# Kernel tuning notes

Measured on AMD Instinct MI355X. Metric: run time of the kernel, lower is better.

Reference implementation:

```python
import jax, jax.numpy as jnp
import numpy as np

H = 128          # hidden_dim
NC = 100000      # num_cst
NV = 100000      # num_val
E = 1600000      # num edges
EPS = 1e-5


def _layernorm(x, g, b):
    mu = x.mean(-1, keepdims=True)
    var = x.var(-1, keepdims=True)
    return (x - mu) / jnp.sqrt(var + EPS) * g + b


def setup_inputs() -> dict:
    key = jax.random.key(0)
    ks = jax.random.split(key, 16)
    s = 0.05
    return {
        "x_val": jax.random.normal(ks[0], (NV, H), jnp.float32),
        "r_cst": jax.random.normal(ks[1], (NC, H), jnp.float32),
        "cst_edges": jax.random.randint(ks[2], (2, E), 0, NC, dtype=jnp.int32),
        "LE": jax.random.randint(ks[3], (E,), 0, 2, dtype=jnp.int32),
        "PE": jax.random.randint(ks[4], (E,), 0, 2, dtype=jnp.int32),
        "num_cst": NC,
        "num_val": NV,
        # cst_send: Linear(H,H,bias) -> ReLU -> Linear(H,4H,no bias) -> LayerNorm(4H)
        "W1": jax.random.normal(ks[5], (H, H), jnp.float32) * s,
        "b1": jax.random.normal(ks[6], (H,), jnp.float32) * s,
        "W2": jax.random.normal(ks[7], (H, 4 * H), jnp.float32) * s,
        "g1": jnp.ones((4 * H,), jnp.float32),
        "bt1": jnp.zeros((4 * H,), jnp.float32),
        # val_rec: Linear(H,H,bias) -> ReLU -> Linear(H,H,no bias) -> LayerNorm(H)
        "W3": jax.random.normal(ks[8], (H, H), jnp.float32) * s,
        "b3": jax.random.normal(ks[9], (H,), jnp.float32) * s,
        "W4": jax.random.normal(ks[10], (H, H), jnp.float32) * s,
        "g2": jnp.ones((H,), jnp.float32),
        "bt2": jnp.zeros((H,), jnp.float32),
    }


def reference(x_val, r_cst, cst_edges, LE, PE, num_cst, num_val,
              W1, b1, W2, g1, bt1, W3, b3, W4, g2, bt2):
    # cst_send MLP: [NC, H] -> [NC, 4H], LayerNorm over 4H, then view as [4*NC, H]
    m = _layernorm(jnp.maximum(r_cst @ W1 + b1, 0.0) @ W2, g1, bt1)
    m = m.reshape(4 * num_cst, H)
    # each edge picks one of the 4 message slots of its constraint
    out_idx = 4 * cst_edges[0] + 2 * LE + PE   # [E]
    in_idx = cst_edges[1]                      # [E]
    msg = m[out_idx]                           # [E, H] gather
    r_val = jax.ops.segment_sum(msg, in_idx, num_segments=num_val)  # [NV, H]
    # val_rec MLP on (x_val + r_val) with residual
    h = x_val + r_val
    return _layernorm(jnp.maximum(h @ W3 + b3, 0.0) @ W4, g2, bt2) + x_val
```

## Files before the change

### kernel.cpp

```cpp
#include <hip/hip_runtime.h>
#include <hip/hip_bf16.h>

#define H 128
#define H4 512
#define BM 16
#define BM2 32

typedef __bf16 bf16x8 __attribute__((ext_vector_type(8)));
typedef float f32x4 __attribute__((ext_vector_type(4)));

__device__ inline f32x4 mfma16(bf16x8 a, bf16x8 b, f32x4 c) {
  return __builtin_amdgcn_mfma_f32_16x16x32_bf16(a, b, c, 0, 0, 0);
}

__global__ __launch_bounds__(256) void pack_kernel(const float* __restrict__ W, int K, int N,
                                                   __bf16* __restrict__ hi,
                                                   __bf16* __restrict__ lo) {
  int idx = blockIdx.x * 256 + threadIdx.x;
  int total = (N >> 4) * (K >> 5) * 64;
  if (idx >= total) return;
  int lane = idx & 63;
  int tile = idx >> 6;
  int KT = K >> 5;
  int nt = tile / KT, kt = tile - nt * KT;
  int col = nt * 16 + (lane & 15);
  int k0 = kt * 32 + (lane >> 4) * 8;
#pragma unroll
  for (int i = 0; i < 8; ++i) {
    float x = W[(long)(k0 + i) * N + col];
    __bf16 h = (__bf16)x;
    hi[(long)idx * 8 + i] = h;
    lo[(long)idx * 8 + i] = (__bf16)(x - (float)h);
  }
}

__global__ __launch_bounds__(256) void copy_kernel(const float4* __restrict__ src,
                                                   float4* __restrict__ dst, int n4) {
  int i = blockIdx.x * 256 + threadIdx.x;
  int stride = gridDim.x * 256;
  for (; i < n4; i += stride) dst[i] = src[i];
}

__device__ inline void split8(const float* p, bf16x8& hi, bf16x8& lo) {
  float4 u = *(const float4*)p, v = *(const float4*)(p + 4);
  float vals[8] = {u.x, u.y, u.z, u.w, v.x, v.y, v.z, v.w};
#pragma unroll
  for (int i = 0; i < 8; ++i) {
    __bf16 hh = (__bf16)vals[i];
    hi[i] = hh;
    lo[i] = (__bf16)(vals[i] - (float)hh);
  }
}

__global__ __launch_bounds__(256) void cst_mlp_mfma(
    const float* __restrict__ r_cst,
    const __bf16* __restrict__ W1h, const __bf16* __restrict__ W1l,
    const float* __restrict__ b1,
    const __bf16* __restrict__ W2h, const __bf16* __restrict__ W2l,
    const float* __restrict__ g1, const float* __restrict__ bt1,
    float* __restrict__ m) {
  __shared__ float As[BM2][132];
  __shared__ float Cs[BM2][132];
  __shared__ float part_s[BM2][4];
  __shared__ float part_q[BM2][4];
  __shared__ float mu_s[BM2], rs_s[BM2];

  const int tid = threadIdx.x;
  const int wave = tid >> 6, lane = tid & 63;
  const long row0 = (long)blockIdx.x * BM2;

  {
    const float4* src = (const float4*)(r_cst + row0 * H);
#pragma unroll
    for (int i = 0; i < 4; ++i) {
      int idx = tid + i * 256;
      int r = idx >> 5, c4 = idx & 31;
      *(float4*)&As[r][c4 * 4] = src[idx];
    }
  }
  __syncthreads();

  const int fr = lane & 15;
  const int fk = (lane >> 4) * 8;
  const int rowb = (lane >> 4) * 4;

  bf16x8 a_hi[2][4], a_lo[2][4];
#pragma unroll
  for (int mt = 0; mt < 2; ++mt)
#pragma unroll
    for (int kt = 0; kt < 4; ++kt) split8(&As[mt * 16 + fr][kt * 32 + fk], a_hi[mt][kt], a_lo[mt][kt]);

#pragma unroll
  for (int t = 0; t < 2; ++t) {
    const int nt = wave * 2 + t;
    f32x4 acc0 = {0.f, 0.f, 0.f, 0.f}, acc1 = {0.f, 0.f, 0.f, 0.f};
#pragma unroll
    for (int kt = 0; kt < 4; ++kt) {
      const long fi = (long)((nt * 4 + kt) * 64 + lane) * 8;
      bf16x8 bh = *(const bf16x8*)(W1h + fi);
      bf16x8 bl = *(const bf16x8*)(W1l + fi);
      acc0 = mfma16(a_hi[0][kt], bh, acc0);
      acc0 = mfma16(a_lo[0][kt], bh, acc0);
      acc0 = mfma16(a_hi[0][kt], bl, acc0);
      acc1 = mfma16(a_hi[1][kt], bh, acc1);
      acc1 = mfma16(a_lo[1][kt], bh, acc1);
      acc1 = mfma16(a_hi[1][kt], bl, acc1);
    }
    const int col = nt * 16 + fr;
    const float bb = b1[col];
#pragma unroll
    for (int r = 0; r < 4; ++r) {
      Cs[rowb + r][col] = fmaxf(acc0[r] + bb, 0.f);
      Cs[16 + rowb + r][col] = fmaxf(acc1[r] + bb, 0.f);
    }
  }
  __syncthreads();

  bf16x8 c_hi[2][4], c_lo[2][4];
#pragma unroll
  for (int mt = 0; mt < 2; ++mt)
#pragma unroll
    for (int kt = 0; kt < 4; ++kt) split8(&Cs[mt * 16 + fr][kt * 32 + fk], c_hi[mt][kt], c_lo[mt][kt]);

  f32x4 d[2][8];
  float ss[2][4], qq[2][4];
#pragma unroll
  for (int mt = 0; mt < 2; ++mt)
#pragma unroll
    for (int r = 0; r < 4; ++r) ss[mt][r] = qq[mt][r] = 0.f;

#pragma unroll
  for (int t = 0; t < 8; ++t) {
    const int nt = wave * 8 + t;
    f32x4 acc0 = {0.f, 0.f, 0.f, 0.f}, acc1 = {0.f, 0.f, 0.f, 0.f};
#pragma unroll
    for (int kt = 0; kt < 4; ++kt) {
      const long fi = (long)((nt * 4 + kt) * 64 + lane) * 8;
      bf16x8 bh = *(const bf16x8*)(W2h + fi);
      bf16x8 bl = *(const bf16x8*)(W2l + fi);
      acc0 = mfma16(c_hi[0][kt], bh, acc0);
      acc0 = mfma16(c_lo[0][kt], bh, acc0);
      acc0 = mfma16(c_hi[0][kt], bl, acc0);
      acc1 = mfma16(c_hi[1][kt], bh, acc1);
      acc1 = mfma16(c_lo[1][kt], bh, acc1);
      acc1 = mfma16(c_hi[1][kt], bl, acc1);
    }
    d[0][t] = acc0;
    d[1][t] = acc1;
#pragma unroll
    for (int r = 0; r < 4; ++r) {
      ss[0][r] += acc0[r];
      qq[0][r] += acc0[r] * acc0[r];
      ss[1][r] += acc1[r];
      qq[1][r] += acc1[r] * acc1[r];
    }
  }

#pragma unroll
  for (int mt = 0; mt < 2; ++mt)
#pragma unroll
    for (int r = 0; r < 4; ++r) {
      float s = ss[mt][r], q = qq[mt][r];
#pragma unroll
      for (int off = 1; off < 16; off <<= 1) {
        s += __shfl_xor(s, off);
        q += __shfl_xor(q, off);
      }
      if (fr == 0) {
        part_s[mt * 16 + rowb + r][wave] = s;
        part_q[mt * 16 + rowb + r][wave] = q;
      }
    }
  __syncthreads();

  if (tid < BM2) {
    float s = part_s[tid][0] + part_s[tid][1] + part_s[tid][2] + part_s[tid][3];
    float q = part_q[tid][0] + part_q[tid][1] + part_q[tid][2] + part_q[tid][3];
    float mu = s * (1.f / H4);
    mu_s[tid] = mu;
    rs_s[tid] = rsqrtf(q * (1.f / H4) - mu * mu + 1e-5f);
  }
  __syncthreads();

#pragma unroll
  for (int t = 0; t < 8; ++t) {
    const int col = (wave * 8 + t) * 16 + fr;
    const float g = g1[col], b = bt1[col];
#pragma unroll
    for (int mt = 0; mt < 2; ++mt) {
#pragma unroll
      for (int r = 0; r < 4; ++r) {
        const int row = mt * 16 + rowb + r;
        m[(row0 + row) * H4 + col] = (d[mt][t][r] - mu_s[row]) * rs_s[row] * g + b;
      }
    }
  }
}

__global__ __launch_bounds__(256) void val_mlp_mfma(
    const float* h, const float* __restrict__ x_val,
    const __bf16* __restrict__ W3h, const __bf16* __restrict__ W3l,
    const float* __restrict__ b3,
    const __bf16* __restrict__ W4h, const __bf16* __restrict__ W4l,
    const float* __restrict__ g2, const float* __restrict__ bt2,
    float* out) {
  __shared__ float As[BM2][132];
  __shared__ float Cs[BM2][132];
  __shared__ float part_s[BM2][4];
  __shared__ float part_q[BM2][4];
  __shared__ float mu_s[BM2], rs_s[BM2];

  const int tid = threadIdx.x;
  const int wave = tid >> 6, lane = tid & 63;
  const long row0 = (long)blockIdx.x * BM2;

  {
    const float4* src = (const float4*)(h + row0 * H);
#pragma unroll
    for (int i = 0; i < 4; ++i) {
      int idx = tid + i * 256;
      int r = idx >> 5, c4 = idx & 31;
      *(float4*)&As[r][c4 * 4] = src[idx];
    }
  }
  __syncthreads();

  const int fr = lane & 15;
  const int fk = (lane >> 4) * 8;
  const int rowb = (lane >> 4) * 4;

  bf16x8 a_hi[2][4], a_lo[2][4];
#pragma unroll
  for (int mt = 0; mt < 2; ++mt)
#pragma unroll
    for (int kt = 0; kt < 4; ++kt) split8(&As[mt * 16 + fr][kt * 32 + fk], a_hi[mt][kt], a_lo[mt][kt]);

#pragma unroll
  for (int t = 0; t < 2; ++t) {
    const int nt = wave * 2 + t;
    f32x4 acc0 = {0.f, 0.f, 0.f, 0.f}, acc1 = {0.f, 0.f, 0.f, 0.f};
#pragma unroll
    for (int kt = 0; kt < 4; ++kt) {
      const long fi = (long)((nt * 4 + kt) * 64 + lane) * 8;
      bf16x8 bh = *(const bf16x8*)(W3h + fi);
      bf16x8 bl = *(const bf16x8*)(W3l + fi);
      acc0 = mfma16(a_hi[0][kt], bh, acc0);
      acc0 = mfma16(a_lo[0][kt], bh, acc0);
      acc0 = mfma16(a_hi[0][kt], bl, acc0);
      acc1 = mfma16(a_hi[1][kt], bh, acc1);
      acc1 = mfma16(a_lo[1][kt], bh, acc1);
      acc1 = mfma16(a_hi[1][kt], bl, acc1);
    }
    const int col = nt * 16 + fr;
    const float bb = b3[col];
#pragma unroll
    for (int r = 0; r < 4; ++r) {
      Cs[rowb + r][col] = fmaxf(acc0[r] + bb, 0.f);
      Cs[16 + rowb + r][col] = fmaxf(acc1[r] + bb, 0.f);
    }
  }
  __syncthreads();

  bf16x8 c_hi[2][4], c_lo[2][4];
#pragma unroll
  for (int mt = 0; mt < 2; ++mt)
#pragma unroll
    for (int kt = 0; kt < 4; ++kt) split8(&Cs[mt * 16 + fr][kt * 32 + fk], c_hi[mt][kt], c_lo[mt][kt]);

  f32x4 d[2][2];
  float ss[2][4], qq[2][4];
#pragma unroll
  for (int mt = 0; mt < 2; ++mt)
#pragma unroll
    for (int r = 0; r < 4; ++r) ss[mt][r] = qq[mt][r] = 0.f;

#pragma unroll
  for (int t = 0; t < 2; ++t) {
    const int nt = wave * 2 + t;
    f32x4 acc0 = {0.f, 0.f, 0.f, 0.f}, acc1 = {0.f, 0.f, 0.f, 0.f};
#pragma unroll
    for (int kt = 0; kt < 4; ++kt) {
      const long fi = (long)((nt * 4 + kt) * 64 + lane) * 8;
      bf16x8 bh = *(const bf16x8*)(W4h + fi);
      bf16x8 bl = *(const bf16x8*)(W4l + fi);
      acc0 = mfma16(c_hi[0][kt], bh, acc0);
      acc0 = mfma16(c_lo[0][kt], bh, acc0);
      acc0 = mfma16(c_hi[0][kt], bl, acc0);
      acc1 = mfma16(c_hi[1][kt], bh, acc1);
      acc1 = mfma16(c_lo[1][kt], bh, acc1);
      acc1 = mfma16(c_hi[1][kt], bl, acc1);
    }
    d[0][t] = acc0;
    d[1][t] = acc1;
#pragma unroll
    for (int r = 0; r < 4; ++r) {
      ss[0][r] += acc0[r];
      qq[0][r] += acc0[r] * acc0[r];
      ss[1][r] += acc1[r];
      qq[1][r] += acc1[r] * acc1[r];
    }
  }

#pragma unroll
  for (int mt = 0; mt < 2; ++mt)
#pragma unroll
    for (int r = 0; r < 4; ++r) {
      float s = ss[mt][r], q = qq[mt][r];
#pragma unroll
      for (int off = 1; off < 16; off <<= 1) {
        s += __shfl_xor(s, off);
        q += __shfl_xor(q, off);
      }
      if (fr == 0) {
        part_s[mt * 16 + rowb + r][wave] = s;
        part_q[mt * 16 + rowb + r][wave] = q;
      }
    }
  __syncthreads();

  if (tid < BM2) {
    float s = part_s[tid][0] + part_s[tid][1] + part_s[tid][2] + part_s[tid][3];
    float q = part_q[tid][0] + part_q[tid][1] + part_q[tid][2] + part_q[tid][3];
    float mu = s * (1.f / H);
    mu_s[tid] = mu;
    rs_s[tid] = rsqrtf(q * (1.f / H) - mu * mu + 1e-5f);
  }
  __syncthreads();

#pragma unroll
  for (int t = 0; t < 2; ++t) {
    const int col = (wave * 2 + t) * 16 + fr;
    const float g = g2[col], b = bt2[col];
#pragma unroll
    for (int mt = 0; mt < 2; ++mt) {
#pragma unroll
      for (int r = 0; r < 4; ++r) {
        const int row = mt * 16 + rowb + r;
        const float xv = x_val[(row0 + row) * H + col];
        out[(row0 + row) * H + col] = (d[mt][t][r] - mu_s[row]) * rs_s[row] * g + b + xv;
      }
    }
  }
}

__global__ __launch_bounds__(256) void cst_mlp_kernel(
    const float* __restrict__ r_cst,
    const float* __restrict__ W1, const float* __restrict__ b1,
    const float* __restrict__ W2, const float* __restrict__ g1,
    const float* __restrict__ bt1, float* __restrict__ m) {
  __shared__ float As[BM][H];
  __shared__ float Cs[BM][H];
  __shared__ float Ds[BM][H4];
  __shared__ float mu_s[BM], rs_s[BM];
  const int tid = threadIdx.x;
  const long row0 = (long)blockIdx.x * BM;
  {
    const float4* src = (const float4*)(r_cst + row0 * H);
    float4* dst = (float4*)&As[0][0];
#pragma unroll
    for (int i = 0; i < 2; ++i) dst[tid + i * 256] = src[tid + i * 256];
  }
  __syncthreads();
  {
    const int j = tid & (H - 1);
    const int r0 = (tid >> 7) * 8;
    float acc[8] = {0, 0, 0, 0, 0, 0, 0, 0};
#pragma unroll 4
    for (int k = 0; k < H; ++k) {
      float w = W1[k * H + j];
#pragma unroll
      for (int r = 0; r < 8; ++r) acc[r] = fmaf(As[r0 + r][k], w, acc[r]);
    }
    float bb = b1[j];
#pragma unroll
    for (int r = 0; r < 8; ++r) Cs[r0 + r][j] = fmaxf(acc[r] + bb, 0.f);
  }
  __syncthreads();
  {
    const int j = tid * 2;
    float acc[BM][2];
#pragma unroll
    for (int r = 0; r < BM; ++r) acc[r][0] = acc[r][1] = 0.f;
    for (int k = 0; k < H; k += 4) {
      float4 c[BM];
#pragma unroll
      for (int r = 0; r < BM; ++r) c[r] = *(const float4*)&Cs[r][k];
#pragma unroll
      for (int kk = 0; kk < 4; ++kk) {
        const float2 w = *(const float2*)&W2[(k + kk) * H4 + j];
#pragma unroll
        for (int r = 0; r < BM; ++r) {
          float cv = (&c[r].x)[kk];
          acc[r][0] = fmaf(cv, w.x, acc[r][0]);
          acc[r][1] = fmaf(cv, w.y, acc[r][1]);
        }
      }
    }
#pragma unroll
    for (int r = 0; r < BM; ++r) {
      Ds[r][j] = acc[r][0];
      Ds[r][j + 1] = acc[r][1];
    }
  }
  __syncthreads();
  {
    const int wv = tid >> 6, lane = tid & 63;
    for (int r = wv * 4; r < wv * 4 + 4; ++r) {
      float s = 0.f, q = 0.f;
      const float4* rowp = (const float4*)&Ds[r][0];
#pragma unroll
      for (int i = 0; i < 2; ++i) {
        float4 v = rowp[lane * 2 + i];
        s += v.x + v.y + v.z + v.w;
        q += v.x * v.x + v.y * v.y + v.z * v.z + v.w * v.w;
      }
#pragma unroll
      for (int off = 32; off; off >>= 1) {
        s += __shfl_xor(s, off);
        q += __shfl_xor(q, off);
      }
      if (lane == 0) {
        float mu = s * (1.f / H4);
        mu_s[r] = mu;
        rs_s[r] = rsqrtf(q * (1.f / H4) - mu * mu + 1e-5f);
      }
    }
  }
  __syncthreads();
  {
    float4* out4 = (float4*)(m + row0 * H4);
    const float4* D4 = (const float4*)&Ds[0][0];
    const float4* g4 = (const float4*)g1;
    const float4* b4 = (const float4*)bt1;
#pragma unroll
    for (int it = 0; it < 8; ++it) {
      int e4 = tid + it * 256;
      int r = e4 >> 7;
      int c4 = e4 & 127;
      float4 v = D4[e4];
      float4 g = g4[c4], b = b4[c4];
      float mu = mu_s[r], rs = rs_s[r];
      float4 o;
      o.x = (v.x - mu) * rs * g.x + b.x;
      o.y = (v.y - mu) * rs * g.y + b.y;
      o.z = (v.z - mu) * rs * g.z + b.z;
      o.w = (v.w - mu) * rs * g.w + b.w;
      out4[e4] = o;
    }
  }
}

__global__ __launch_bounds__(256) void val_mlp_kernel(
    const float* h, const float* __restrict__ x_val,
    const float* __restrict__ W3, const float* __restrict__ b3,
    const float* __restrict__ W4, const float* __restrict__ g2,
    const float* __restrict__ bt2, float* out) {
  __shared__ float As[BM][H];
  __shared__ float Cs[BM][H];
  __shared__ float Ds[BM][H];
  __shared__ float mu_s[BM], rs_s[BM];
  const int tid = threadIdx.x;
  const long row0 = (long)blockIdx.x * BM;
  {
    const float4* src = (const float4*)(h + row0 * H);
    float4* dst = (float4*)&As[0][0];
#pragma unroll
    for (int i = 0; i < 2; ++i) dst[tid + i * 256] = src[tid + i * 256];
  }
  __syncthreads();
  const int j = tid & (H - 1);
  const int r0 = (tid >> 7) * 8;
  {
    float acc[8] = {0, 0, 0, 0, 0, 0, 0, 0};
#pragma unroll 4
    for (int k = 0; k < H; ++k) {
      float w = W3[k * H + j];
#pragma unroll
      for (int r = 0; r < 8; ++r) acc[r] = fmaf(As[r0 + r][k], w, acc[r]);
    }
    float bb = b3[j];
#pragma unroll
    for (int r = 0; r < 8; ++r) Cs[r0 + r][j] = fmaxf(acc[r] + bb, 0.f);
  }
  __syncthreads();
  {
    float acc[8] = {0, 0, 0, 0, 0, 0, 0, 0};
#pragma unroll 4
    for (int k = 0; k < H; ++k) {
      float w = W4[k * H + j];
#pragma unroll
      for (int r = 0; r < 8; ++r) acc[r] = fmaf(Cs[r0 + r][k], w, acc[r]);
    }
#pragma unroll
    for (int r = 0; r < 8; ++r) Ds[r0 + r][j] = acc[r];
  }
  __syncthreads();
  {
    const int wv = tid >> 6, lane = tid & 63;
    for (int r = wv * 4; r < wv * 4 + 4; ++r) {
      float2 v = *(const float2*)&Ds[r][lane * 2];
      float s = v.x + v.y, q = v.x * v.x + v.y * v.y;
#pragma unroll
      for (int off = 32; off; off >>= 1) {
        s += __shfl_xor(s, off);
        q += __shfl_xor(q, off);
      }
      if (lane == 0) {
        float mu = s * (1.f / H);
        mu_s[r] = mu;
        rs_s[r] = rsqrtf(q * (1.f / H) - mu * mu + 1e-5f);
      }
    }
  }
  __syncthreads();
  {
    float4* out4 = (float4*)(out + row0 * H);
    const float4* x4 = (const float4*)(x_val + row0 * H);
    const float4* D4 = (const float4*)&Ds[0][0];
    const float4* g4 = (const float4*)g2;
    const float4* b4 = (const float4*)bt2;
#pragma unroll
    for (int it = 0; it < 2; ++it) {
      int e4 = tid + it * 256;
      int r = e4 >> 5;
      int c4 = e4 & 31;
      float4 v = D4[e4];
      float4 g = g4[c4], b = b4[c4], xv = x4[e4];
      float mu = mu_s[r], rs = rs_s[r];
      float4 o;
      o.x = (v.x - mu) * rs * g.x + b.x + xv.x;
      o.y = (v.y - mu) * rs * g.y + b.y + xv.y;
      o.z = (v.z - mu) * rs * g.z + b.z + xv.z;
      o.w = (v.w - mu) * rs * g.w + b.w + xv.w;
      out4[e4] = o;
    }
  }
}

__global__ __launch_bounds__(256) void count_kernel(const int* __restrict__ e_in,
                                                    int* __restrict__ cnt, int nE) {
  int i = blockIdx.x * 256 + threadIdx.x;
  if (i < nE) atomicAdd(&cnt[e_in[i]], 1);
}

__device__ inline int wave_incl_scan(int x) {
#pragma unroll
  for (int off = 1; off < 64; off <<= 1) {
    int y = __shfl_up(x, off);
    if ((threadIdx.x & 63) >= off) x += y;
  }
  return x;
}

__global__ __launch_bounds__(256) void scan1_kernel(const int* __restrict__ cnt,
                                                    int* __restrict__ offs,
                                                    int* __restrict__ bsums, int n) {
  int i = blockIdx.x * 256 + threadIdx.x;
  int v = (i < n) ? cnt[i] : 0;
  int incl = wave_incl_scan(v);
  __shared__ int wsum[4];
  int wv = threadIdx.x >> 6, lane = threadIdx.x & 63;
  if (lane == 63) wsum[wv] = incl;
  __syncthreads();
  int add = 0;
  for (int w = 0; w < wv; ++w) add += wsum[w];
  if (i < n) offs[i] = incl - v + add;
  if (threadIdx.x == 255) bsums[blockIdx.x] = incl + add;
}

__global__ __launch_bounds__(1024) void scan2_kernel(int* __restrict__ bsums, int nb,
                                                     int* __restrict__ offs, int n, int total) {
  __shared__ int s[1024];
  int t = threadIdx.x;
  int orig = (t < nb) ? bsums[t] : 0;
  s[t] = orig;
  __syncthreads();
  for (int off = 1; off < 1024; off <<= 1) {
    int v = (t >= off) ? s[t - off] : 0;
    __syncthreads();
    s[t] += v;
    __syncthreads();
  }
  if (t < nb) bsums[t] = s[t] - orig;
  if (t == 0) offs[n] = total;
}

__global__ __launch_bounds__(256) void scan3_kernel(int* __restrict__ offs,
                                                    const int* __restrict__ bsums, int n) {
  int i = blockIdx.x * 256 + threadIdx.x;
  if (i < n) offs[i] += bsums[blockIdx.x];
}

__global__ __launch_bounds__(256) void fill_kernel(
    const int* __restrict__ e_out, const int* __restrict__ e_in,
    const int* __restrict__ LE, const int* __restrict__ PE,
    const int* __restrict__ offs, int* __restrict__ cnt2,
    int* __restrict__ msg_row, int nE) {
  int e = blockIdx.x * 256 + threadIdx.x;
  if (e >= nE) return;
  int v = e_in[e];
  int pos = offs[v] + atomicAdd(&cnt2[v], 1);
  msg_row[pos] = 4 * e_out[e] + 2 * LE[e] + PE[e];
}

__global__ __launch_bounds__(256) void gather_kernel(
    const float* __restrict__ m, const float* __restrict__ x_val,
    const int* __restrict__ offs, const int* __restrict__ msg_row,
    float* __restrict__ h, int nv) {
  int v = blockIdx.x * 4 + (threadIdx.x >> 6);
  if (v >= nv) return;
  int lane = threadIdx.x & 63;
  int beg = offs[v], end = offs[v + 1];
  float2 acc = *(const float2*)(x_val + (long)v * H + lane * 2);
  int p = beg;
  for (; p + 3 < end; p += 4) {
    int r0 = msg_row[p];
    int r1 = msg_row[p + 1];
    int r2 = msg_row[p + 2];
    int r3 = msg_row[p + 3];
    float2 a = *(const float2*)(m + (long)r0 * H + lane * 2);
    float2 b = *(const float2*)(m + (long)r1 * H + lane * 2);
    float2 c = *(const float2*)(m + (long)r2 * H + lane * 2);
    float2 d = *(const float2*)(m + (long)r3 * H + lane * 2);
    acc.x += (a.x + b.x) + (c.x + d.x);
    acc.y += (a.y + b.y) + (c.y + d.y);
  }
  for (; p < end; ++p) {
    int r0 = msg_row[p];
    float2 a = *(const float2*)(m + (long)r0 * H + lane * 2);
    acc.x += a.x;
    acc.y += a.y;
  }
  *(float2*)(h + (long)v * H + lane * 2) = acc;
}

__global__ __launch_bounds__(256) void scatter_kernel(
    const float* __restrict__ m, const int* __restrict__ e_out,
    const int* __restrict__ e_in, const int* __restrict__ LE,
    const int* __restrict__ PE, float* h, int nE) {
  int t = blockIdx.x * 256 + threadIdx.x;
  int edge = t >> 5;
  if (edge >= nE) return;
  int lane = t & 31;
  int c0 = e_out[edge];
  int c1 = e_in[edge];
  int oi = 4 * c0 + 2 * LE[edge] + PE[edge];
  float4 v = *(const float4*)(m + (long)oi * H + lane * 4);
  float* dst = h + (long)c1 * H + lane * 4;
  unsafeAtomicAdd(dst + 0, v.x);
  unsafeAtomicAdd(dst + 1, v.y);
  unsafeAtomicAdd(dst + 2, v.z);
  unsafeAtomicAdd(dst + 3, v.w);
}

extern "C" void kernel_launch(void* const* d_in, const int* in_sizes, int n_in,
                              void* d_out, int out_size, void* d_ws, size_t ws_size,
                              hipStream_t stream) {
  const float* x_val = (const float*)d_in[0];
  const float* r_cst = (const float*)d_in[1];
  const int* edges  = (const int*)d_in[2];
  const int* LE     = (const int*)d_in[3];
  const int* PE     = (const int*)d_in[4];
  const float* W1  = (const float*)d_in[7];
  const float* b1  = (const float*)d_in[8];
  const float* W2  = (const float*)d_in[9];
  const float* g1  = (const float*)d_in[10];
  const float* bt1 = (const float*)d_in[11];
  const float* W3  = (const float*)d_in[12];
  const float* b3  = (const float*)d_in[13];
  const float* W4  = (const float*)d_in[14];
  const float* g2  = (const float*)d_in[15];
  const float* bt2 = (const float*)d_in[16];

  const int NV = in_sizes[0] / H;
  const int NC = in_sizes[1] / H;
  const int nE = in_sizes[3];

  float* out  = (float*)d_out;
  float* mbuf = (float*)d_ws;

  const size_t mbytes = (size_t)4 * NC * H * sizeof(float);
  int* offs  = (int*)((char*)d_ws + mbytes);
  int* cnt   = offs + (NV + 1);
  int* cnt2  = cnt + NV;
  int* bsums = cnt2 + NV;
  int* msg_row = bsums + 1024;
  const size_t csr_bytes = ((size_t)(NV + 1) + NV + NV + 1024 + nE) * sizeof(int);
  const size_t need_csr = mbytes + csr_bytes;

  const size_t pack_off = (need_csr + 63) & ~(size_t)63;
  __bf16* W1h = (__bf16*)((char*)d_ws + pack_off);
  __bf16* W1l = W1h + 16384;
  __bf16* W2h = W1l + 16384;
  __bf16* W2l = W2h + 65536;
  __bf16* W3h = W2l + 65536;
  __bf16* W3l = W3h + 16384;
  __bf16* W4h = W3l + 16384;
  __bf16* W4l = W4h + 16384;
  const size_t need_mfma = pack_off + (size_t)(2 * (16384 * 3 + 65536)) * sizeof(__bf16);

  const int nb = (NV + 255) / 256;
  const bool csr_ok = (ws_size >= need_csr) && (nb <= 1024);
  const bool mfma_ok = csr_ok && (ws_size >= need_mfma) && (NC % BM2 == 0) && (NV % BM2 == 0);

  if (mfma_ok) {
    pack_kernel<<<8, 256, 0, stream>>>(W1, H, H, W1h, W1l);
    pack_kernel<<<32, 256, 0, stream>>>(W2, H, H4, W2h, W2l);
    pack_kernel<<<8, 256, 0, stream>>>(W3, H, H, W3h, W3l);
    pack_kernel<<<8, 256, 0, stream>>>(W4, H, H, W4h, W4l);
    cst_mlp_mfma<<<NC / BM2, 256, 0, stream>>>(r_cst, W1h, W1l, b1, W2h, W2l, g1, bt1, mbuf);
  } else {
    cst_mlp_kernel<<<NC / BM, 256, 0, stream>>>(r_cst, W1, b1, W2, g1, bt1, mbuf);
  }

  if (csr_ok) {
    hipMemsetAsync(cnt, 0, (size_t)NV * sizeof(int), stream);
    hipMemsetAsync(cnt2, 0, (size_t)NV * sizeof(int), stream);
    count_kernel<<<(nE + 255) / 256, 256, 0, stream>>>(edges + nE, cnt, nE);
    scan1_kernel<<<nb, 256, 0, stream>>>(cnt, offs, bsums, NV);
    scan2_kernel<<<1, 1024, 0, stream>>>(bsums, nb, offs, NV, nE);
    scan3_kernel<<<nb, 256, 0, stream>>>(offs, bsums, NV);
    fill_kernel<<<(nE + 255) / 256, 256, 0, stream>>>(edges, edges + nE, LE, PE, offs, cnt2,
                                                      msg_row, nE);
    gather_kernel<<<(NV + 3) / 4, 256, 0, stream>>>(mbuf, x_val, offs, msg_row, out, NV);
  } else {
    copy_kernel<<<2048, 256, 0, stream>>>((const float4*)x_val, (float4*)out, NV * H / 4);
    scatter_kernel<<<(nE * 32 + 255) / 256, 256, 0, stream>>>(mbuf, edges, edges + nE, LE, PE,
                                                              out, nE);
  }

  if (mfma_ok) {
    val_mlp_mfma<<<NV / BM2, 256, 0, stream>>>(out, x_val, W3h, W3l, b3, W4h, W4l, g2, bt2, out);
  } else {
    val_mlp_kernel<<<NV / BM, 256, 0, stream>>>(out, x_val, W3, b3, W4, g2, bt2, out);
  }
}
```

Before: 653.7 us.

## Load MLP inputs directly to registers, stage bf16 splits in LDS, widen gather

Both MLP kernels now read A fragments straight from global memory, with no fp32 LDS staging pass and one fewer barrier. The hidden activation is split into bf16 hi/lo when it is written to LDS, and the second GEMM reads those fragments from LDS. This drops the register-held c_hi/c_lo arrays so a 3-blocks-per-CU launch bound can apply. The gather kernel splits each wave into two halves that take alternating edges with float4 loads and combine through a cross-half shuffle, which adds shuffle cost and idles the upper half at the final store.

```diff
diff --git a/kernel.cpp b/kernel.cpp
--- a/kernel.cpp
+++ b/kernel.cpp
@@ -5,6 +5,7 @@
 #define H4 512
 #define BM 16
 #define BM2 32
+#define CPAD 136
 
 typedef __bf16 bf16x8 __attribute__((ext_vector_type(8)));
 typedef float f32x4 __attribute__((ext_vector_type(4)));
@@ -52,15 +53,15 @@
   }
 }
 
-__global__ __launch_bounds__(256) void cst_mlp_mfma(
+__global__ __launch_bounds__(256, 3) void cst_mlp_mfma(
     const float* __restrict__ r_cst,
     const __bf16* __restrict__ W1h, const __bf16* __restrict__ W1l,
     const float* __restrict__ b1,
     const __bf16* __restrict__ W2h, const __bf16* __restrict__ W2l,
     const float* __restrict__ g1, const float* __restrict__ bt1,
     float* __restrict__ m) {
-  __shared__ float As[BM2][132];
-  __shared__ float Cs[BM2][132];
+  __shared__ __bf16 Ch[BM2][CPAD];
+  __shared__ __bf16 Cl[BM2][CPAD];
   __shared__ float part_s[BM2][4];
   __shared__ float part_q[BM2][4];
   __shared__ float mu_s[BM2], rs_s[BM2];
@@ -69,26 +70,17 @@
   const int wave = tid >> 6, lane = tid & 63;
   const long row0 = (long)blockIdx.x * BM2;
 
-  {
-    const float4* src = (const float4*)(r_cst + row0 * H);
-#pragma unroll
-    for (int i = 0; i < 4; ++i) {
-      int idx = tid + i * 256;
-      int r = idx >> 5, c4 = idx & 31;
-      *(float4*)&As[r][c4 * 4] = src[idx];
-    }
-  }
-  __syncthreads();
-
   const int fr = lane & 15;
-  const int fk = (lane >> 4) * 8;
+  const int fkb = (lane >> 4) * 8;
   const int rowb = (lane >> 4) * 4;
 
   bf16x8 a_hi[2][4], a_lo[2][4];
 #pragma unroll
-  for (int mt = 0; mt < 2; ++mt)
-#pragma unroll
-    for (int kt = 0; kt < 4; ++kt) split8(&As[mt * 16 + fr][kt * 32 + fk], a_hi[mt][kt], a_lo[mt][kt]);
+  for (int mt = 0; mt < 2; ++mt) {
+    const float* arow = r_cst + (row0 + mt * 16 + fr) * H;
+#pragma unroll
+    for (int kt = 0; kt < 4; ++kt) split8(arow + kt * 32 + fkb, a_hi[mt][kt], a_lo[mt][kt]);
+  }
 
 #pragma unroll
   for (int t = 0; t < 2; ++t) {
@@ -110,17 +102,16 @@
     const float bb = b1[col];
 #pragma unroll
     for (int r = 0; r < 4; ++r) {
-      Cs[rowb + r][col] = fmaxf(acc0[r] + bb, 0.f);
-      Cs[16 + rowb + r][col] = fmaxf(acc1[r] + bb, 0.f);
-    }
-  }
-  __syncthreads();
-
-  bf16x8 c_hi[2][4], c_lo[2][4];
-#pragma unroll
-  for (int mt = 0; mt < 2; ++mt)
-#pragma unroll
-    for (int kt = 0; kt < 4; ++kt) split8(&Cs[mt * 16 + fr][kt * 32 + fk], c_hi[mt][kt], c_lo[mt][kt]);
+      float v0 = fmaxf(acc0[r] + bb, 0.f);
+      float v1 = fmaxf(acc1[r] + bb, 0.f);
+      __bf16 h0 = (__bf16)v0, h1 = (__bf16)v1;
+      Ch[rowb + r][col] = h0;
+      Cl[rowb + r][col] = (__bf16)(v0 - (float)h0);
+      Ch[16 + rowb + r][col] = h1;
+      Cl[16 + rowb + r][col] = (__bf16)(v1 - (float)h1);
+    }
+  }
+  __syncthreads();
 
   f32x4 d[2][8];
   float ss[2][4], qq[2][4];
@@ -138,12 +129,16 @@
       const long fi = (long)((nt * 4 + kt) * 64 + lane) * 8;
       bf16x8 bh = *(const bf16x8*)(W2h + fi);
       bf16x8 bl = *(const bf16x8*)(W2l + fi);
-      acc0 = mfma16(c_hi[0][kt], bh, acc0);
-      acc0 = mfma16(c_lo[0][kt], bh, acc0);
-      acc0 = mfma16(c_hi[0][kt], bl, acc0);
-      acc1 = mfma16(c_hi[1][kt], bh, acc1);
-      acc1 = mfma16(c_lo[1][kt], bh, acc1);
-      acc1 = mfma16(c_hi[1][kt], bl, acc1);
+      bf16x8 ch0 = *(const bf16x8*)&Ch[fr][kt * 32 + fkb];
+      bf16x8 cl0 = *(const bf16x8*)&Cl[fr][kt * 32 + fkb];
+      bf16x8 ch1 = *(const bf16x8*)&Ch[16 + fr][kt * 32 + fkb];
+      bf16x8 cl1 = *(const bf16x8*)&Cl[16 + fr][kt * 32 + fkb];
+      acc0 = mfma16(ch0, bh, acc0);
+      acc0 = mfma16(cl0, bh, acc0);
+      acc0 = mfma16(ch0, bl, acc0);
+      acc1 = mfma16(ch1, bh, acc1);
+      acc1 = mfma16(cl1, bh, acc1);
+      acc1 = mfma16(ch1, bl, acc1);
     }
     d[0][t] = acc0;
     d[1][t] = acc1;
@@ -197,15 +192,15 @@
   }
 }
 
-__global__ __launch_bounds__(256) void val_mlp_mfma(
+__global__ __launch_bounds__(256, 3) void val_mlp_mfma(
     const float* h, const float* __restrict__ x_val,
     const __bf16* __restrict__ W3h, const __bf16* __restrict__ W3l,
     const float* __restrict__ b3,
     const __bf16* __restrict__ W4h, const __bf16* __restrict__ W4l,
     const float* __restrict__ g2, const float* __restrict__ bt2,
     float* out) {
-  __shared__ float As[BM2][132];
-  __shared__ float Cs[BM2][132];
+  __shared__ __bf16 Ch[BM2][CPAD];
+  __shared__ __bf16 Cl[BM2][CPAD];
   __shared__ float part_s[BM2][4];
   __shared__ float part_q[BM2][4];
   __shared__ float mu_s[BM2], rs_s[BM2];
@@ -214,26 +209,17 @@
   const int wave = tid >> 6, lane = tid & 63;
   const long row0 = (long)blockIdx.x * BM2;
 
-  {
-    const float4* src = (const float4*)(h + row0 * H);
-#pragma unroll
-    for (int i = 0; i < 4; ++i) {
-      int idx = tid + i * 256;
-      int r = idx >> 5, c4 = idx & 31;
-      *(float4*)&As[r][c4 * 4] = src[idx];
-    }
-  }
-  __syncthreads();
-
   const int fr = lane & 15;
-  const int fk = (lane >> 4) * 8;
+  const int fkb = (lane >> 4) * 8;
   const int rowb = (lane >> 4) * 4;
 
   bf16x8 a_hi[2][4], a_lo[2][4];
 #pragma unroll
-  for (int mt = 0; mt < 2; ++mt)
-#pragma unroll
-    for (int kt = 0; kt < 4; ++kt) split8(&As[mt * 16 + fr][kt * 32 + fk], a_hi[mt][kt], a_lo[mt][kt]);
+  for (int mt = 0; mt < 2; ++mt) {
+    const float* arow = h + (row0 + mt * 16 + fr) * H;
+#pragma unroll
+    for (int kt = 0; kt < 4; ++kt) split8(arow + kt * 32 + fkb, a_hi[mt][kt], a_lo[mt][kt]);
+  }
 
 #pragma unroll
   for (int t = 0; t < 2; ++t) {
@@ -255,17 +241,16 @@
     const float bb = b3[col];
 #pragma unroll
     for (int r = 0; r < 4; ++r) {
-      Cs[rowb + r][col] = fmaxf(acc0[r] + bb, 0.f);
-      Cs[16 + rowb + r][col] = fmaxf(acc1[r] + bb, 0.f);
-    }
-  }
-  __syncthreads();
-
-  bf16x8 c_hi[2][4], c_lo[2][4];
-#pragma unroll
-  for (int mt = 0; mt < 2; ++mt)
-#pragma unroll
-    for (int kt = 0; kt < 4; ++kt) split8(&Cs[mt * 16 + fr][kt * 32 + fk], c_hi[mt][kt], c_lo[mt][kt]);
+      float v0 = fmaxf(acc0[r] + bb, 0.f);
+      float v1 = fmaxf(acc1[r] + bb, 0.f);
+      __bf16 h0 = (__bf16)v0, h1 = (__bf16)v1;
+      Ch[rowb + r][col] = h0;
+      Cl[rowb + r][col] = (__bf16)(v0 - (float)h0);
+      Ch[16 + rowb + r][col] = h1;
+      Cl[16 + rowb + r][col] = (__bf16)(v1 - (float)h1);
+    }
+  }
+  __syncthreads();
 
   f32x4 d[2][2];
   float ss[2][4], qq[2][4];
@@ -283,12 +268,16 @@
       const long fi = (long)((nt * 4 + kt) * 64 + lane) * 8;
       bf16x8 bh = *(const bf16x8*)(W4h + fi);
       bf16x8 bl = *(const bf16x8*)(W4l + fi);
-      acc0 = mfma16(c_hi[0][kt], bh, acc0);
-      acc0 = mfma16(c_lo[0][kt], bh, acc0);
-      acc0 = mfma16(c_hi[0][kt], bl, acc0);
-      acc1 = mfma16(c_hi[1][kt], bh, acc1);
-      acc1 = mfma16(c_lo[1][kt], bh, acc1);
-      acc1 = mfma16(c_hi[1][kt], bl, acc1);
+      bf16x8 ch0 = *(const bf16x8*)&Ch[fr][kt * 32 + fkb];
+      bf16x8 cl0 = *(const bf16x8*)&Cl[fr][kt * 32 + fkb];
+      bf16x8 ch1 = *(const bf16x8*)&Ch[16 + fr][kt * 32 + fkb];
+      bf16x8 cl1 = *(const bf16x8*)&Cl[16 + fr][kt * 32 + fkb];
+      acc0 = mfma16(ch0, bh, acc0);
+      acc0 = mfma16(cl0, bh, acc0);
+      acc0 = mfma16(ch0, bl, acc0);
+      acc1 = mfma16(ch1, bh, acc1);
+      acc1 = mfma16(cl1, bh, acc1);
+      acc1 = mfma16(ch1, bl, acc1);
     }
     d[0][t] = acc0;
     d[1][t] = acc1;
@@ -610,28 +599,40 @@
   int v = blockIdx.x * 4 + (threadIdx.x >> 6);
   if (v >= nv) return;
   int lane = threadIdx.x & 63;
+  int half = lane >> 5, li = lane & 31;
   int beg = offs[v], end = offs[v + 1];
-  float2 acc = *(const float2*)(x_val + (long)v * H + lane * 2);
-  int p = beg;
-  for (; p + 3 < end; p += 4) {
+  float4 acc = {0.f, 0.f, 0.f, 0.f};
+  int p = beg + half;
+  for (; p + 2 < end; p += 4) {
     int r0 = msg_row[p];
-    int r1 = msg_row[p + 1];
-    int r2 = msg_row[p + 2];
-    int r3 = msg_row[p + 3];
-    float2 a = *(const float2*)(m + (long)r0 * H + lane * 2);
-    float2 b = *(const float2*)(m + (long)r1 * H + lane * 2);
-    float2 c = *(const float2*)(m + (long)r2 * H + lane * 2);
-    float2 d = *(const float2*)(m + (long)r3 * H + lane * 2);
-    acc.x += (a.x + b.x) + (c.x + d.x);
-    acc.y += (a.y + b.y) + (c.y + d.y);
-  }
-  for (; p < end; ++p) {
+    int r1 = msg_row[p + 2];
+    float4 a = *(const float4*)(m + (long)r0 * H + li * 4);
+    float4 b = *(const float4*)(m + (long)r1 * H + li * 4);
+    acc.x += a.x + b.x;
+    acc.y += a.y + b.y;
+    acc.z += a.z + b.z;
+    acc.w += a.w + b.w;
+  }
+  if (p < end) {
     int r0 = msg_row[p];
-    float2 a = *(const float2*)(m + (long)r0 * H + lane * 2);
+    float4 a = *(const float4*)(m + (long)r0 * H + li * 4);
     acc.x += a.x;
     acc.y += a.y;
-  }
-  *(float2*)(h + (long)v * H + lane * 2) = acc;
+    acc.z += a.z;
+    acc.w += a.w;
+  }
+  acc.x += __shfl_xor(acc.x, 32);
+  acc.y += __shfl_xor(acc.y, 32);
+  acc.z += __shfl_xor(acc.z, 32);
+  acc.w += __shfl_xor(acc.w, 32);
+  if (half == 0) {
+    float4 xv = *(const float4*)(x_val + (long)v * H + li * 4);
+    acc.x += xv.x;
+    acc.y += xv.y;
+    acc.z += xv.z;
+    acc.w += xv.w;
+    *(float4*)(h + (long)v * H + li * 4) = acc;
+  }
 }
 
 __global__ __launch_bounds__(256) void scatter_kernel(
```

After: 635.7 us. -2.7%, faster.
